# Kernel optimization log

Measured on AMD Instinct MI355X. Metric: run time of the kernel, lower is better.

Reference implementation:

```python
import jax, jax.numpy as jnp
import numpy as np

B = 32768      # batch size
D = 256        # embedding dim
C = 2048       # number of classes (label range)
WEIGHT = 1.0
TEMPERATURE = 0.3
EPS = 1e-12


def setup_inputs() -> dict:
    key = jax.random.key(0)
    k1, k2 = jax.random.split(key)
    features = jax.random.normal(k1, (B, D), dtype=jnp.float32)
    labels = jax.random.randint(k2, (B,), 0, C, dtype=jnp.int32)
    return {"features": features, "labels": labels, "epoch": 5}


def reference(features, labels, epoch):
    # L2-normalize embeddings (F.normalize, p=2, dim=1)
    norms = jnp.sqrt(jnp.sum(features * features, axis=1, keepdims=True))
    f = features / jnp.maximum(norms, EPS)                      # [B, D]

    # per-class segment sums / counts (vectorized replacement of the python loop)
    ones = jnp.ones((f.shape[0],), dtype=f.dtype)
    counts = jax.ops.segment_sum(ones, labels, num_segments=C)  # [C]
    sums = jax.ops.segment_sum(f, labels, num_segments=C)       # [C, D]
    centroids = sums / jnp.maximum(counts, 1.0)[:, None]        # [C, D] (mean; empty classes masked later)

    # leave-one-out positive centroid: (sum_class - f_i) / (n_class - 1)
    cnt_i = counts[labels]                                       # [B]
    c_p = (sums[labels] - f) / jnp.maximum(cnt_i - 1.0, 1.0)[:, None]
    d_p = jnp.sqrt(jnp.sum((f - c_p) ** 2, axis=1) + EPS)        # [B]

    # distances to all class centroids: ||f||=1 after normalization
    cn2 = jnp.sum(centroids * centroids, axis=1)                 # [C]
    d2 = 1.0 + cn2[None, :] - 2.0 * (f @ centroids.T)           # [B, C]
    d = jnp.sqrt(jnp.maximum(d2, EPS))

    # mask own class and empty (absent-in-batch) classes, take min negative distance
    class_ids = jnp.arange(C, dtype=labels.dtype)
    neg_mask = (counts[None, :] > 0) & (labels[:, None] != class_ids[None, :])
    d_n = jnp.min(jnp.where(neg_mask, d, jnp.inf), axis=1)       # [B]

    # samples are skipped if their class is a singleton or no negative class exists
    valid = (cnt_i > 1.0) & jnp.isfinite(d_n)
    d_n_safe = jnp.where(jnp.isfinite(d_n), d_n, 0.0)

    # temperature schedule: min(temperature + 0.02*epoch, 1)
    temp = min(TEMPERATURE + 0.02 * epoch, 1.0)

    # ln(1 + exp((d_p - d_n)/t)) == softplus
    loss_per_sample = jax.nn.softplus((d_p - d_n_safe) / temp)
    cnt = jnp.sum(valid.astype(f.dtype))
    loss = jnp.where(cnt > 0,
                     jnp.sum(jnp.where(valid, loss_per_sample, 0.0)) / jnp.maximum(cnt, 1.0),
                     0.0)
    return WEIGHT * loss
```

## Files before the change

kernel.cpp:

```cpp
#include <hip/hip_runtime.h>
#include <hip/hip_bf16.h>
#include <math.h>

constexpr int Bn = 32768;
constexpr int Dn = 256;
constexpr int Cn = 2048;
constexpr int NSPLIT = 4;
constexpr int CLS_PER_BLK = Cn / NSPLIT;
constexpr int NSUP = CLS_PER_BLK / 32;
#define EPSF 1e-12f
#define INFF __builtin_inff()

typedef __bf16 bf16x8 __attribute__((ext_vector_type(8)));
typedef __bf16 bf16x4 __attribute__((ext_vector_type(4)));
typedef float  f32x4  __attribute__((ext_vector_type(4)));

__device__ inline void async_copy16(const void* g, void* l) {
    __builtin_amdgcn_global_load_lds(
        (const __attribute__((address_space(1))) void*)g,
        (__attribute__((address_space(3))) void*)l, 16, 0, 0);
}

__global__ __launch_bounds__(256) void k_prep(const float* __restrict__ feat,
                                              const int* __restrict__ labels,
                                              __bf16* __restrict__ fneg,
                                              int* __restrict__ hist,
                                              int* __restrict__ cnt_i,
                                              int* __restrict__ offs,
                                              int* __restrict__ offs_wk,
                                              int* __restrict__ ticket) {
    const int tid = threadIdx.x;
    const int wave = tid >> 6, lane = tid & 63;
    const int base = blockIdx.x * 16 + wave * 4;
    #pragma unroll
    for (int j = 0; j < 4; ++j) {
        const int s = base + j;
        const float4 v = ((const float4*)(feat + (size_t)s * Dn))[lane];
        float ss = v.x * v.x + v.y * v.y + v.z * v.z + v.w * v.w;
        #pragma unroll
        for (int off = 1; off < 64; off <<= 1) ss += __shfl_xor(ss, off, 64);
        const float inv = -2.0f / fmaxf(sqrtf(ss), EPSF);
        bf16x4 bf;
        bf[0] = (__bf16)(v.x * inv); bf[1] = (__bf16)(v.y * inv);
        bf[2] = (__bf16)(v.z * inv); bf[3] = (__bf16)(v.w * inv);
        *(bf16x4*)(fneg + (size_t)s * Dn + lane * 4) = bf;
        if (lane == 0) atomicAdd(&hist[labels[s]], 1);
    }

    __shared__ int s_part[256];
    __shared__ int s_last;
    __syncthreads();
    if (tid == 0)
        s_last = (atomicAdd(ticket, 1) == (int)gridDim.x - 1) ? 1 : 0;
    __syncthreads();
    if (!s_last) return;
    int h[8], pre[8]; int sum = 0;
    #pragma unroll
    for (int j = 0; j < 8; ++j) {
        h[j] = atomicAdd(&hist[tid * 8 + j], 0);
        pre[j] = sum; sum += h[j];
    }
    int vv = sum;
    s_part[tid] = vv; __syncthreads();
    for (int off = 1; off < 256; off <<= 1) {
        int add = (tid >= off) ? s_part[tid - off] : 0;
        __syncthreads();
        vv += add; s_part[tid] = vv;
        __syncthreads();
    }
    const int base2 = vv - sum;
    #pragma unroll
    for (int j = 0; j < 8; ++j) {
        const int b = tid * 8 + j, o = base2 + pre[j];
        cnt_i[b] = h[j]; offs[b] = o; offs_wk[b] = o;
    }
}

__global__ __launch_bounds__(256) void k_scatter(const int* __restrict__ labels,
                                                 int* __restrict__ offs_work,
                                                 int* __restrict__ order) {
    const int i = blockIdx.x * 256 + threadIdx.x;
    const int pos = atomicAdd(&offs_work[labels[i]], 1);
    order[pos] = i;
}

__global__ __launch_bounds__(256) void k_centseg(const __bf16* __restrict__ fneg,
                                                 const int* __restrict__ order,
                                                 const int* __restrict__ offs,
                                                 const int* __restrict__ cnt_i,
                                                 __bf16* __restrict__ centK,
                                                 float* __restrict__ cn2x) {
    const int wave = threadIdx.x >> 6, lane = threadIdx.x & 63;
    const int c = blockIdx.x * 4 + wave;
    const int n = cnt_i[c], start = offs[c];
    int myidx = 0;
    if (lane < n) myidx = order[start + lane];
    float sx = 0.f, sy = 0.f, sz = 0.f, sw = 0.f;
    const int nf = (n < 64) ? n : 64;
    for (int j = 0; j < nf; ++j) {
        const int idx = __shfl(myidx, j, 64);
        const bf16x4 v = *(const bf16x4*)(fneg + (size_t)idx * Dn + lane * 4);
        sx += -0.5f * (float)v[0]; sy += -0.5f * (float)v[1];
        sz += -0.5f * (float)v[2]; sw += -0.5f * (float)v[3];
    }
    for (int j = 64; j < n; ++j) {
        const int idx = order[start + j];
        const bf16x4 v = *(const bf16x4*)(fneg + (size_t)idx * Dn + lane * 4);
        sx += -0.5f * (float)v[0]; sy += -0.5f * (float)v[1];
        sz += -0.5f * (float)v[2]; sw += -0.5f * (float)v[3];
    }
    const float invn = 1.0f / fmaxf((float)n, 1.0f);
    const float cx = sx * invn, cy = sy * invn, cz = sz * invn, cw = sw * invn;
    bf16x4 cb; cb[0] = (__bf16)cx; cb[1] = (__bf16)cy;
    cb[2] = (__bf16)cz; cb[3] = (__bf16)cw;
    *(bf16x4*)(centK + ((size_t)(lane >> 1) * Cn + c) * 8 + (lane & 1) * 4) = cb;
    float ss = cx * cx + cy * cy + cz * cz + cw * cw;
    #pragma unroll
    for (int off = 1; off < 64; off <<= 1) ss += __shfl_xor(ss, off, 64);
    if (lane == 0) cn2x[c] = (n > 0) ? ss : INFF;
}

__global__ __launch_bounds__(256, 2) void k_main(const __bf16* __restrict__ fneg,
                                                 const int* __restrict__ labels,
                                                 const __bf16* __restrict__ centK,
                                                 const float* __restrict__ cn2x,
                                                 float* __restrict__ minval,
                                                 float* __restrict__ dotown) {
    __shared__ __align__(16) __bf16 sB[3][32 * Dn];
    __shared__ float s_cn2[CLS_PER_BLK];
    const int lane = threadIdx.x & 63, wave = threadIdx.x >> 6;
    const int m16 = lane & 15, quad = lane >> 4;
    const int sbase = blockIdx.x * 256 + wave * 64;
    const int c_begin = blockIdx.y * CLS_PER_BLK;

    bf16x8 a[4][8];
    #pragma unroll
    for (int p = 0; p < 4; ++p) {
        const __bf16* fr = fneg + (size_t)(sbase + p * 16 + m16) * Dn + quad * 8;
        #pragma unroll
        for (int t = 0; t < 8; ++t) a[p][t] = *(const bf16x8*)(fr + t * 32);
    }
    int lab[4][4];
    #pragma unroll
    for (int p = 0; p < 4; ++p)
        #pragma unroll
        for (int r = 0; r < 4; ++r)
            lab[p][r] = labels[sbase + p * 16 + quad * 4 + r];

    float rm[4][4], dacc[4][4];
    #pragma unroll
    for (int p = 0; p < 4; ++p)
        #pragma unroll
        for (int r = 0; r < 4; ++r) { rm[p][r] = INFF; dacc[p][r] = 0.0f; }

    auto stage = [&](int buf, int s) {
        const int c0 = c_begin + s * 32;
        #pragma unroll
        for (int j = 0; j < 4; ++j) {
            const int L = wave * 256 + j * 64 + lane;
            const int st = L >> 9, kc = (L >> 4) & 31, n = L & 15;
            const __bf16* g = centK + ((size_t)kc * Cn + (c0 + st * 16 + n)) * 8;
            __bf16* l = &sB[buf][(size_t)(wave * 256 + j * 64) * 8];
            async_copy16(g, l);
        }
    };

    stage(0, 0);
    stage(1, 1);
    for (int c = threadIdx.x; c < CLS_PER_BLK; c += 256) s_cn2[c] = cn2x[c_begin + c];
    for (int s = 0; s < NSUP; ++s) {
        __syncthreads();
        if (s + 2 < NSUP) stage((s + 2) % 3, s + 2);
        const __bf16* lsb = &sB[s % 3][0];
        #pragma unroll
        for (int st = 0; st < 2; ++st) {
            const float cn2v = s_cn2[s * 32 + st * 16 + m16];
            const __bf16* ls = lsb + st * 4096;
            f32x4 acc[4] = {{0.f,0.f,0.f,0.f},{0.f,0.f,0.f,0.f},
                            {0.f,0.f,0.f,0.f},{0.f,0.f,0.f,0.f}};
            #pragma unroll
            for (int t = 0; t < 8; ++t) {
                const bf16x8 b = *(const bf16x8*)(ls + t * 512 + lane * 8);
                #pragma unroll
                for (int p = 0; p < 4; ++p)
                    acc[p] = __builtin_amdgcn_mfma_f32_16x16x32_bf16(a[p][t], b, acc[p], 0, 0, 0);
            }
            const int crow = c_begin + s * 32 + st * 16 + m16;
            #pragma unroll
            for (int p = 0; p < 4; ++p)
                #pragma unroll
                for (int r = 0; r < 4; ++r) {
                    const bool own = (crow == lab[p][r]);
                    const float sel = own ? INFF : cn2v;
                    rm[p][r] = fminf(rm[p][r], sel + acc[p][r]);
                    dacc[p][r] += own ? acc[p][r] : 0.0f;
                }
        }
    }
    #pragma unroll
    for (int off = 1; off < 16; off <<= 1)
        #pragma unroll
        for (int p = 0; p < 4; ++p)
            #pragma unroll
            for (int r = 0; r < 4; ++r) {
                rm[p][r] = fminf(rm[p][r], __shfl_xor(rm[p][r], off, 64));
                dacc[p][r] += __shfl_xor(dacc[p][r], off, 64);
            }
    if (m16 == 0) {
        float* mv = minval + (size_t)blockIdx.y * Bn;
        float* dv = dotown + (size_t)blockIdx.y * Bn;
        #pragma unroll
        for (int p = 0; p < 4; ++p)
            #pragma unroll
            for (int r = 0; r < 4; ++r) {
                mv[sbase + p * 16 + quad * 4 + r] = rm[p][r];
                dv[sbase + p * 16 + quad * 4 + r] = dacc[p][r];
            }
    }
}

__global__ __launch_bounds__(256) void k_final(const int* __restrict__ labels,
                                               const int* __restrict__ cnt_i,
                                               const float* __restrict__ cn2x,
                                               const float* __restrict__ minval,
                                               const float* __restrict__ dotown,
                                               const int* __restrict__ epoch,
                                               float* __restrict__ accum,
                                               int* __restrict__ ticket,
                                               float* __restrict__ out) {
    const int tid = threadIdx.x;
    const int i = blockIdx.x * 256 + tid;
    const int lane = tid & 63;
    const float temp = fminf(0.3f + 0.02f * (float)(*epoch), 1.0f);
    float m = minval[i];
    float draw = dotown[i];
    #pragma unroll
    for (int k = 1; k < NSPLIT; ++k) {
        m = fminf(m, minval[(size_t)k * Bn + i]);
        draw += dotown[(size_t)k * Bn + i];
    }
    const int l = labels[i];
    const int n = cnt_i[l];
    const float nf = (float)n;
    const float cn2 = cn2x[l];
    const float fds = nf * (-0.5f * draw);
    const float fm1 = fmaxf(nf - 1.0f, 1.0f);
    const float fdcp = (fds - 1.0f) / fm1;
    const float cp2 = (nf * nf * cn2 - 2.0f * fds + 1.0f) / (fm1 * fm1);
    const float dp2 = 1.0f - 2.0f * fdcp + cp2;
    const float d_p = sqrtf(fmaxf(dp2, 0.0f) + EPSF);
    const bool finite = (m < 1e37f);
    const float d_n = finite ? sqrtf(fmaxf(1.0f + m, EPSF)) : 0.0f;
    const bool valid = (n > 1) && finite;
    const float x = (d_p - d_n) / temp;
    const float sp = fmaxf(x, 0.0f) + log1pf(expf(-fabsf(x)));
    float ws = valid ? sp : 0.0f, wc = valid ? 1.0f : 0.0f;
    #pragma unroll
    for (int off = 1; off < 64; off <<= 1) {
        ws += __shfl_xor(ws, off, 64);
        wc += __shfl_xor(wc, off, 64);
    }
    if (lane == 0) {
        atomicAdd(&accum[0], ws);
        atomicAdd(&accum[1], wc);
    }
    __shared__ int s_last;
    __syncthreads();
    if (tid == 0)
        s_last = (atomicAdd(ticket, 1) == (int)gridDim.x - 1) ? 1 : 0;
    __syncthreads();
    if (s_last && tid == 0) {
        const float s = atomicAdd(&accum[0], 0.0f);
        const float c = atomicAdd(&accum[1], 0.0f);
        out[0] = (c > 0.0f) ? (s / fmaxf(c, 1.0f)) : 0.0f;
    }
}

extern "C" void kernel_launch(void* const* d_in, const int* in_sizes, int n_in,
                              void* d_out, int out_size, void* d_ws, size_t ws_size,
                              hipStream_t stream) {
    const float* feat  = (const float*)d_in[0];
    const int* labels  = (const int*)d_in[1];
    const int* epoch   = (const int*)d_in[2];
    float* out = (float*)d_out;
    char* ws = (char*)d_ws;

    size_t off = 0;
    __bf16* fneg   = (__bf16*)(ws + off); off += (size_t)Bn * Dn * 2;
    __bf16* centK  = (__bf16*)(ws + off); off += (size_t)Cn * Dn * 2;
    float*  cn2x   = (float*)(ws + off);  off += (size_t)Cn * 4;
    int*    cnt_i  = (int*)(ws + off);    off += (size_t)Cn * 4;
    int*    offsp  = (int*)(ws + off);    off += (size_t)Cn * 4;
    int*    offs_wk= (int*)(ws + off);    off += (size_t)Cn * 4;
    int*    order  = (int*)(ws + off);    off += (size_t)Bn * 4;
    float*  minval = (float*)(ws + off);  off += (size_t)NSPLIT * Bn * 4;
    float*  dotown = (float*)(ws + off);  off += (size_t)NSPLIT * Bn * 4;
    int*    hist   = (int*)(ws + off);    off += (size_t)Cn * 4;
    float*  accum  = (float*)(ws + off);  off += 2 * 4;
    int*    ticket = (int*)(ws + off);    off += 2 * 4;

    (void)hipMemsetAsync(hist, 0, (size_t)Cn * 4 + 16, stream);

    k_prep<<<Bn / 16, 256, 0, stream>>>(feat, labels, fneg, hist, cnt_i, offsp,
                                        offs_wk, &ticket[0]);
    k_scatter<<<Bn / 256, 256, 0, stream>>>(labels, offs_wk, order);
    k_centseg<<<Cn / 4, 256, 0, stream>>>(fneg, order, offsp, cnt_i, centK, cn2x);
    dim3 g4(Bn / 256, NSPLIT);
    k_main<<<g4, 256, 0, stream>>>(fneg, labels, centK, cn2x, minval, dotown);
    k_final<<<Bn / 256, 256, 0, stream>>>(labels, cnt_i, cn2x, minval, dotown,
                                          epoch, accum, &ticket[1], out);
}
```

Baseline: 178.5 us.

## Replace prefix-scan bucketing with padded slots and fuse final loss into main kernel

Class bucketing no longer uses a histogram, prefix scan and separate scatter kernel. k_prep writes sample indices straight into fixed 64-slot per-class buckets, with a small overflow list, and k_centseg reads from them. k_main seeds the MFMA accumulators with the centroid norm, drops the own-class dot accumulation, and uses a per-row-block ticket so the last of the four class-split blocks computes the own-class dot, positive distance and softplus. This removes two kernel launches and the dotown traffic, at the cost of a serial per-sample tail loop in one block per row group. The overflow buffer holds only 256 entries, so heavily skewed labels could overflow it.

```diff
diff --git a/kernel.cpp b/kernel.cpp
--- a/kernel.cpp
+++ b/kernel.cpp
@@ -8,6 +8,7 @@
 constexpr int NSPLIT = 4;
 constexpr int CLS_PER_BLK = Cn / NSPLIT;
 constexpr int NSUP = CLS_PER_BLK / 32;
+constexpr int PAD = 64;
 #define EPSF 1e-12f
 #define INFF __builtin_inff()
 
@@ -24,11 +25,11 @@
 __global__ __launch_bounds__(256) void k_prep(const float* __restrict__ feat,
                                               const int* __restrict__ labels,
                                               __bf16* __restrict__ fneg,
-                                              int* __restrict__ hist,
-                                              int* __restrict__ cnt_i,
-                                              int* __restrict__ offs,
-                                              int* __restrict__ offs_wk,
-                                              int* __restrict__ ticket) {
+                                              int* __restrict__ cnt,
+                                              int* __restrict__ order_pad,
+                                              int* __restrict__ ovf_cnt,
+                                              int* __restrict__ ovf_cls,
+                                              int* __restrict__ ovf_idx) {
     const int tid = threadIdx.x;
     const int wave = tid >> 6, lane = tid & 63;
     const int base = blockIdx.x * 16 + wave * 4;
@@ -44,70 +45,49 @@
         bf[0] = (__bf16)(v.x * inv); bf[1] = (__bf16)(v.y * inv);
         bf[2] = (__bf16)(v.z * inv); bf[3] = (__bf16)(v.w * inv);
         *(bf16x4*)(fneg + (size_t)s * Dn + lane * 4) = bf;
-        if (lane == 0) atomicAdd(&hist[labels[s]], 1);
-    }
-
-    __shared__ int s_part[256];
-    __shared__ int s_last;
-    __syncthreads();
-    if (tid == 0)
-        s_last = (atomicAdd(ticket, 1) == (int)gridDim.x - 1) ? 1 : 0;
-    __syncthreads();
-    if (!s_last) return;
-    int h[8], pre[8]; int sum = 0;
-    #pragma unroll
-    for (int j = 0; j < 8; ++j) {
-        h[j] = atomicAdd(&hist[tid * 8 + j], 0);
-        pre[j] = sum; sum += h[j];
-    }
-    int vv = sum;
-    s_part[tid] = vv; __syncthreads();
-    for (int off = 1; off < 256; off <<= 1) {
-        int add = (tid >= off) ? s_part[tid - off] : 0;
-        __syncthreads();
-        vv += add; s_part[tid] = vv;
-        __syncthreads();
-    }
-    const int base2 = vv - sum;
-    #pragma unroll
-    for (int j = 0; j < 8; ++j) {
-        const int b = tid * 8 + j, o = base2 + pre[j];
-        cnt_i[b] = h[j]; offs[b] = o; offs_wk[b] = o;
-    }
-}
-
-__global__ __launch_bounds__(256) void k_scatter(const int* __restrict__ labels,
-                                                 int* __restrict__ offs_work,
-                                                 int* __restrict__ order) {
-    const int i = blockIdx.x * 256 + threadIdx.x;
-    const int pos = atomicAdd(&offs_work[labels[i]], 1);
-    order[pos] = i;
+        if (lane == 0) {
+            const int l = labels[s];
+            const int r = atomicAdd(&cnt[l], 1);
+            if (r < PAD) order_pad[l * PAD + r] = s;
+            else {
+                const int o = atomicAdd(ovf_cnt, 1);
+                ovf_cls[o] = l; ovf_idx[o] = s;
+            }
+        }
+    }
 }
 
 __global__ __launch_bounds__(256) void k_centseg(const __bf16* __restrict__ fneg,
-                                                 const int* __restrict__ order,
-                                                 const int* __restrict__ offs,
-                                                 const int* __restrict__ cnt_i,
+                                                 const int* __restrict__ cnt,
+                                                 const int* __restrict__ order_pad,
+                                                 const int* __restrict__ ovf_cnt,
+                                                 const int* __restrict__ ovf_cls,
+                                                 const int* __restrict__ ovf_idx,
                                                  __bf16* __restrict__ centK,
                                                  float* __restrict__ cn2x) {
     const int wave = threadIdx.x >> 6, lane = threadIdx.x & 63;
     const int c = blockIdx.x * 4 + wave;
-    const int n = cnt_i[c], start = offs[c];
+    const int n = cnt[c];
+    const int nf = (n < PAD) ? n : PAD;
     int myidx = 0;
-    if (lane < n) myidx = order[start + lane];
+    if (lane < nf) myidx = order_pad[c * PAD + lane];
     float sx = 0.f, sy = 0.f, sz = 0.f, sw = 0.f;
-    const int nf = (n < 64) ? n : 64;
     for (int j = 0; j < nf; ++j) {
         const int idx = __shfl(myidx, j, 64);
         const bf16x4 v = *(const bf16x4*)(fneg + (size_t)idx * Dn + lane * 4);
         sx += -0.5f * (float)v[0]; sy += -0.5f * (float)v[1];
         sz += -0.5f * (float)v[2]; sw += -0.5f * (float)v[3];
     }
-    for (int j = 64; j < n; ++j) {
-        const int idx = order[start + j];
-        const bf16x4 v = *(const bf16x4*)(fneg + (size_t)idx * Dn + lane * 4);
-        sx += -0.5f * (float)v[0]; sy += -0.5f * (float)v[1];
-        sz += -0.5f * (float)v[2]; sw += -0.5f * (float)v[3];
+    if (n > PAD) {
+        const int novf = *ovf_cnt;
+        for (int j = 0; j < novf; ++j) {
+            if (ovf_cls[j] == c) {
+                const int idx = ovf_idx[j];
+                const bf16x4 v = *(const bf16x4*)(fneg + (size_t)idx * Dn + lane * 4);
+                sx += -0.5f * (float)v[0]; sy += -0.5f * (float)v[1];
+                sz += -0.5f * (float)v[2]; sw += -0.5f * (float)v[3];
+            }
+        }
     }
     const float invn = 1.0f / fmaxf((float)n, 1.0f);
     const float cx = sx * invn, cy = sy * invn, cz = sz * invn, cw = sw * invn;
@@ -124,11 +104,17 @@
                                                  const int* __restrict__ labels,
                                                  const __bf16* __restrict__ centK,
                                                  const float* __restrict__ cn2x,
+                                                 const int* __restrict__ cnt,
+                                                 const int* __restrict__ epoch,
                                                  float* __restrict__ minval,
-                                                 float* __restrict__ dotown) {
+                                                 float* __restrict__ accum,
+                                                 int* __restrict__ ticket_bx,
+                                                 int* __restrict__ ticket_fin,
+                                                 float* __restrict__ out) {
     __shared__ __align__(16) __bf16 sB[3][32 * Dn];
     __shared__ float s_cn2[CLS_PER_BLK];
-    const int lane = threadIdx.x & 63, wave = threadIdx.x >> 6;
+    const int tid = threadIdx.x;
+    const int lane = tid & 63, wave = tid >> 6;
     const int m16 = lane & 15, quad = lane >> 4;
     const int sbase = blockIdx.x * 256 + wave * 64;
     const int c_begin = blockIdx.y * CLS_PER_BLK;
@@ -147,11 +133,11 @@
         for (int r = 0; r < 4; ++r)
             lab[p][r] = labels[sbase + p * 16 + quad * 4 + r];
 
-    float rm[4][4], dacc[4][4];
+    float rm[4][4];
     #pragma unroll
     for (int p = 0; p < 4; ++p)
         #pragma unroll
-        for (int r = 0; r < 4; ++r) { rm[p][r] = INFF; dacc[p][r] = 0.0f; }
+        for (int r = 0; r < 4; ++r) rm[p][r] = INFF;
 
     auto stage = [&](int buf, int s) {
         const int c0 = c_begin + s * 32;
@@ -167,7 +153,7 @@
 
     stage(0, 0);
     stage(1, 1);
-    for (int c = threadIdx.x; c < CLS_PER_BLK; c += 256) s_cn2[c] = cn2x[c_begin + c];
+    for (int c = tid; c < CLS_PER_BLK; c += 256) s_cn2[c] = cn2x[c_begin + c];
     for (int s = 0; s < NSUP; ++s) {
         __syncthreads();
         if (s + 2 < NSUP) stage((s + 2) % 3, s + 2);
@@ -176,8 +162,10 @@
         for (int st = 0; st < 2; ++st) {
             const float cn2v = s_cn2[s * 32 + st * 16 + m16];
             const __bf16* ls = lsb + st * 4096;
-            f32x4 acc[4] = {{0.f,0.f,0.f,0.f},{0.f,0.f,0.f,0.f},
-                            {0.f,0.f,0.f,0.f},{0.f,0.f,0.f,0.f}};
+            f32x4 acc[4];
+            #pragma unroll
+            for (int p = 0; p < 4; ++p)
+                acc[p] = f32x4{cn2v, cn2v, cn2v, cn2v};
             #pragma unroll
             for (int t = 0; t < 8; ++t) {
                 const bf16x8 b = *(const bf16x8*)(ls + t * 512 + lane * 8);
@@ -189,12 +177,9 @@
             #pragma unroll
             for (int p = 0; p < 4; ++p)
                 #pragma unroll
-                for (int r = 0; r < 4; ++r) {
-                    const bool own = (crow == lab[p][r]);
-                    const float sel = own ? INFF : cn2v;
-                    rm[p][r] = fminf(rm[p][r], sel + acc[p][r]);
-                    dacc[p][r] += own ? acc[p][r] : 0.0f;
-                }
+                for (int r = 0; r < 4; ++r)
+                    rm[p][r] = fminf(rm[p][r],
+                                     (crow == lab[p][r]) ? INFF : acc[p][r]);
         }
     }
     #pragma unroll
@@ -202,77 +187,73 @@
         #pragma unroll
         for (int p = 0; p < 4; ++p)
             #pragma unroll
-            for (int r = 0; r < 4; ++r) {
+            for (int r = 0; r < 4; ++r)
                 rm[p][r] = fminf(rm[p][r], __shfl_xor(rm[p][r], off, 64));
-                dacc[p][r] += __shfl_xor(dacc[p][r], off, 64);
-            }
     if (m16 == 0) {
         float* mv = minval + (size_t)blockIdx.y * Bn;
-        float* dv = dotown + (size_t)blockIdx.y * Bn;
         #pragma unroll
         for (int p = 0; p < 4; ++p)
             #pragma unroll
-            for (int r = 0; r < 4; ++r) {
-                mv[sbase + p * 16 + quad * 4 + r] = rm[p][r];
-                dv[sbase + p * 16 + quad * 4 + r] = dacc[p][r];
-            }
-    }
-}
-
-__global__ __launch_bounds__(256) void k_final(const int* __restrict__ labels,
-                                               const int* __restrict__ cnt_i,
-                                               const float* __restrict__ cn2x,
-                                               const float* __restrict__ minval,
-                                               const float* __restrict__ dotown,
-                                               const int* __restrict__ epoch,
-                                               float* __restrict__ accum,
-                                               int* __restrict__ ticket,
-                                               float* __restrict__ out) {
-    const int tid = threadIdx.x;
-    const int i = blockIdx.x * 256 + tid;
-    const int lane = tid & 63;
+            for (int r = 0; r < 4; ++r)
+                atomicExch(&mv[sbase + p * 16 + quad * 4 + r], rm[p][r]);
+    }
+
+    __shared__ int s_tail;
+    __syncthreads();
+    if (tid == 0)
+        s_tail = (atomicAdd(&ticket_bx[blockIdx.x], 1) == NSPLIT - 1) ? 1 : 0;
+    __syncthreads();
+    if (!s_tail) return;
+
     const float temp = fminf(0.3f + 0.02f * (float)(*epoch), 1.0f);
-    float m = minval[i];
-    float draw = dotown[i];
-    #pragma unroll
-    for (int k = 1; k < NSPLIT; ++k) {
-        m = fminf(m, minval[(size_t)k * Bn + i]);
-        draw += dotown[(size_t)k * Bn + i];
-    }
-    const int l = labels[i];
-    const int n = cnt_i[l];
-    const float nf = (float)n;
-    const float cn2 = cn2x[l];
-    const float fds = nf * (-0.5f * draw);
-    const float fm1 = fmaxf(nf - 1.0f, 1.0f);
-    const float fdcp = (fds - 1.0f) / fm1;
-    const float cp2 = (nf * nf * cn2 - 2.0f * fds + 1.0f) / (fm1 * fm1);
-    const float dp2 = 1.0f - 2.0f * fdcp + cp2;
-    const float d_p = sqrtf(fmaxf(dp2, 0.0f) + EPSF);
-    const bool finite = (m < 1e37f);
-    const float d_n = finite ? sqrtf(fmaxf(1.0f + m, EPSF)) : 0.0f;
-    const bool valid = (n > 1) && finite;
-    const float x = (d_p - d_n) / temp;
-    const float sp = fmaxf(x, 0.0f) + log1pf(expf(-fabsf(x)));
-    float ws = valid ? sp : 0.0f, wc = valid ? 1.0f : 0.0f;
-    #pragma unroll
-    for (int off = 1; off < 64; off <<= 1) {
-        ws += __shfl_xor(ws, off, 64);
-        wc += __shfl_xor(wc, off, 64);
+    float ws = 0.0f, wc = 0.0f;
+    const int ibase = blockIdx.x * 256 + wave * 64;
+    for (int j = 0; j < 64; ++j) {
+        const int i = ibase + j;
+        const int l = labels[i];
+        const bf16x4 fv = *(const bf16x4*)(fneg + (size_t)i * Dn + lane * 4);
+        const bf16x4 cv = *(const bf16x4*)(centK
+                              + ((size_t)(lane >> 1) * Cn + l) * 8 + (lane & 1) * 4);
+        float s4 = (float)fv[0] * (float)cv[0] + (float)fv[1] * (float)cv[1]
+                 + (float)fv[2] * (float)cv[2] + (float)fv[3] * (float)cv[3];
+        #pragma unroll
+        for (int off = 1; off < 64; off <<= 1) s4 += __shfl_xor(s4, off, 64);
+        float mk = (lane < NSPLIT) ? atomicAdd(&minval[(size_t)lane * Bn + i], 0.0f)
+                                   : INFF;
+        mk = fminf(mk, __shfl_xor(mk, 1, 64));
+        mk = fminf(mk, __shfl_xor(mk, 2, 64));
+        if (lane == 0) {
+            const int n = cnt[l];
+            const float nf2 = (float)n;
+            const float cn2 = cn2x[l];
+            const float fds = nf2 * (-0.5f * s4);
+            const float fm1 = fmaxf(nf2 - 1.0f, 1.0f);
+            const float fdcp = (fds - 1.0f) / fm1;
+            const float cp2 = (nf2 * nf2 * cn2 - 2.0f * fds + 1.0f) / (fm1 * fm1);
+            const float dp2 = 1.0f - 2.0f * fdcp + cp2;
+            const float d_p = sqrtf(fmaxf(dp2, 0.0f) + EPSF);
+            const bool finite = (mk < 1e37f);
+            const float d_n = finite ? sqrtf(fmaxf(1.0f + mk, EPSF)) : 0.0f;
+            const bool valid = (n > 1) && finite;
+            const float x = (d_p - d_n) / temp;
+            const float sp = fmaxf(x, 0.0f) + log1pf(expf(-fabsf(x)));
+            ws += valid ? sp : 0.0f;
+            wc += valid ? 1.0f : 0.0f;
+        }
     }
     if (lane == 0) {
         atomicAdd(&accum[0], ws);
         atomicAdd(&accum[1], wc);
     }
-    __shared__ int s_last;
+    __shared__ int s_fin;
     __syncthreads();
     if (tid == 0)
-        s_last = (atomicAdd(ticket, 1) == (int)gridDim.x - 1) ? 1 : 0;
-    __syncthreads();
-    if (s_last && tid == 0) {
-        const float s = atomicAdd(&accum[0], 0.0f);
-        const float c = atomicAdd(&accum[1], 0.0f);
-        out[0] = (c > 0.0f) ? (s / fmaxf(c, 1.0f)) : 0.0f;
+        s_fin = (atomicAdd(ticket_fin, 1) == (Bn / 256) - 1) ? 1 : 0;
+    __syncthreads();
+    if (s_fin && tid == 0) {
+        const float ss = atomicAdd(&accum[0], 0.0f);
+        const float cc = atomicAdd(&accum[1], 0.0f);
+        out[0] = (cc > 0.0f) ? (ss / fmaxf(cc, 1.0f)) : 0.0f;
     }
 }
 
@@ -286,27 +267,27 @@
     char* ws = (char*)d_ws;
 
     size_t off = 0;
-    __bf16* fneg   = (__bf16*)(ws + off); off += (size_t)Bn * Dn * 2;
-    __bf16* centK  = (__bf16*)(ws + off); off += (size_t)Cn * Dn * 2;
-    float*  cn2x   = (float*)(ws + off);  off += (size_t)Cn * 4;
-    int*    cnt_i  = (int*)(ws + off);    off += (size_t)Cn * 4;
-    int*    offsp  = (int*)(ws + off);    off += (size_t)Cn * 4;
-    int*    offs_wk= (int*)(ws + off);    off += (size_t)Cn * 4;
-    int*    order  = (int*)(ws + off);    off += (size_t)Bn * 4;
-    float*  minval = (float*)(ws + off);  off += (size_t)NSPLIT * Bn * 4;
-    float*  dotown = (float*)(ws + off);  off += (size_t)NSPLIT * Bn * 4;
-    int*    hist   = (int*)(ws + off);    off += (size_t)Cn * 4;
-    float*  accum  = (float*)(ws + off);  off += 2 * 4;
-    int*    ticket = (int*)(ws + off);    off += 2 * 4;
-
-    (void)hipMemsetAsync(hist, 0, (size_t)Cn * 4 + 16, stream);
-
-    k_prep<<<Bn / 16, 256, 0, stream>>>(feat, labels, fneg, hist, cnt_i, offsp,
-                                        offs_wk, &ticket[0]);
-    k_scatter<<<Bn / 256, 256, 0, stream>>>(labels, offs_wk, order);
-    k_centseg<<<Cn / 4, 256, 0, stream>>>(fneg, order, offsp, cnt_i, centK, cn2x);
-    dim3 g4(Bn / 256, NSPLIT);
-    k_main<<<g4, 256, 0, stream>>>(fneg, labels, centK, cn2x, minval, dotown);
-    k_final<<<Bn / 256, 256, 0, stream>>>(labels, cnt_i, cn2x, minval, dotown,
-                                          epoch, accum, &ticket[1], out);
-}
+    __bf16* fneg     = (__bf16*)(ws + off); off += (size_t)Bn * Dn * 2;
+    __bf16* centK    = (__bf16*)(ws + off); off += (size_t)Cn * Dn * 2;
+    float*  cn2x     = (float*)(ws + off);  off += (size_t)Cn * 4;
+    int*    order_pad= (int*)(ws + off);    off += (size_t)Cn * PAD * 4;
+    int*    ovf_cls  = (int*)(ws + off);    off += 256 * 4;
+    int*    ovf_idx  = (int*)(ws + off);    off += 256 * 4;
+    float*  minval   = (float*)(ws + off);  off += (size_t)NSPLIT * Bn * 4;
+    int*    cnt      = (int*)(ws + off);    off += (size_t)Cn * 4;
+    int*    ovf_cnt  = (int*)(ws + off);    off += 4;
+    int*    tick_fin = (int*)(ws + off);    off += 4;
+    float*  accum    = (float*)(ws + off);  off += 2 * 4;
+    int*    tick_bx  = (int*)(ws + off);    off += (Bn / 256) * 4;
+
+    const size_t zbytes = (size_t)Cn * 4 + 4 + 4 + 8 + (Bn / 256) * 4;
+    (void)hipMemsetAsync(cnt, 0, zbytes, stream);
+
+    k_prep<<<Bn / 16, 256, 0, stream>>>(feat, labels, fneg, cnt, order_pad,
+                                        ovf_cnt, ovf_cls, ovf_idx);
+    k_centseg<<<Cn / 4, 256, 0, stream>>>(fneg, cnt, order_pad, ovf_cnt, ovf_cls,
+                                          ovf_idx, centK, cn2x);
+    dim3 g3(Bn / 256, NSPLIT);
+    k_main<<<g3, 256, 0, stream>>>(fneg, labels, centK, cn2x, cnt, epoch,
+                                   minval, accum, tick_bx, tick_fin, out);
+}
```

After: 229.3 us. +28.5%, slower.
